# Kernel tuning notes

Hardware: AMD Instinct MI355X
Metric: run time of the kernel (lower is better)

Reference implementation:

```python
import jax, jax.numpy as jnp
import numpy as np

CUTOFF = 5.0
P = 6               # envelope polynomial power
NUM_RBF = 6
NUM_SBF = 7
EMBED = 128
TYPE_EMBED = 64
OUT_EMBED = 256
INT_EMBED = 64      # angle_int_embed_size
BASIS_EMBED = 8
N_BLOCKS = 4
N_DENSE_OUT = 3
N_RES_BEFORE = 1
N_RES_AFTER = 2
N_SPECIES = 16
NUM_TARGETS = 1
N_ATOMS = 4096
N_EDGES = 65536
N_TRIPLETS = 524288

# first 6 positive roots of spherical Bessel j_l, l = 0..6
BESSEL_ZEROS = np.array([
    [3.141593, 6.283185, 9.424778, 12.566371, 15.707963, 18.849556],
    [4.493409, 7.725252, 10.904122, 14.066194, 17.220755, 20.371303],
    [5.763459, 9.095011, 12.322941, 15.514603, 18.689036, 21.853874],
    [6.987932, 10.417119, 13.698023, 16.923621, 20.121806, 23.304247],
    [8.182561, 11.704907, 15.039665, 18.301256, 21.525418, 24.727566],
    [9.355812, 12.966530, 16.354710, 19.653152, 22.904551, 26.126750],
    [10.512835, 14.207392, 17.647975, 20.983463, 24.262768, 27.507868]], dtype=np.float32)

act = jax.nn.silu  # swish


def envelope(x):
    a = -(P + 1) * (P + 2) / 2.0
    b = float(P * (P + 2))
    c = -P * (P + 1) / 2.0
    env = 1.0 / x + a * x ** (P - 1) + b * x ** P + c * x ** (P + 1)
    return jnp.where(x < 1.0, env, 0.0)


def radial_bessel(d):
    # d: (E,) -> (E, NUM_RBF)
    x = d / CUTOFF
    n = jnp.arange(1, NUM_RBF + 1, dtype=jnp.float32)
    return np.float32(np.sqrt(2.0 / CUTOFF)) * envelope(x)[:, None] * jnp.sin(jnp.pi * n[None, :] * x[:, None])


def spherical_basis(d_kj, angles, triplet_mask):
    # d_kj: (T,), angles: (T,) -> (T, NUM_SBF * NUM_RBF)
    x = jnp.maximum(d_kj / CUTOFF, 1e-6)
    env = envelope(x)
    zeros = jnp.asarray(BESSEL_ZEROS)
    radial = []
    for l in range(NUM_SBF):
        a = zeros[l][None, :] * x[:, None]           # (T, NUM_RBF)
        j0 = jnp.sin(a) / a
        if l == 0:
            radial.append(j0)
            continue
        j1 = jnp.sin(a) / a ** 2 - jnp.cos(a) / a
        jm2, jm1 = j0, j1
        for ll in range(2, l + 1):
            jm2, jm1 = jm1, (2 * ll - 1) / a * jm1 - jm2
        radial.append(jm1)
    radial = jnp.stack(radial, axis=1)               # (T, NUM_SBF, NUM_RBF)
    ct = jnp.cos(angles)
    Pl = [jnp.ones_like(ct), ct]
    for l in range(2, NUM_SBF):
        Pl.append(((2 * l - 1) * ct * Pl[l - 1] - (l - 1) * Pl[l - 2]) / l)
    sph = jnp.stack([np.float32(np.sqrt((2 * l + 1) / (4.0 * np.pi))) * Pl[l] for l in range(NUM_SBF)], axis=1)  # (T, NUM_SBF)
    sbf = (env[:, None, None] * radial * sph[:, :, None]).reshape(-1, NUM_SBF * NUM_RBF)
    return jnp.where(triplet_mask[:, None], sbf, 0.0)


def _forward(distances, angles, species_embed, emb_rbf_w, emb_rbf_b, emb_dense_w, emb_dense_b,
             out_rbf_w, out_up_w, out_dense_w, out_dense_b, out_final_w,
             int_ji_w, int_ji_b, int_kj_w, int_kj_b, int_rbf1_w, int_rbf2_w, int_down_w,
             int_sbf1_w, int_sbf2_w, int_up_w, int_res1_w, int_res1_b, int_skip_w, int_skip_b,
             int_res2_w, int_res2_b,
             species, idx_i, idx_j, reduce_to_ji, expand_to_kj, edge_mask, triplet_mask):
    n_particles = species.shape[0]
    n_edges = distances.shape[0]
    d = jnp.where(edge_mask, distances, 2.0 * CUTOFF)       # masked edges -> env = 0
    rbf = radial_bessel(d)                                  # (E, 6)
    sbf = spherical_basis(d[expand_to_kj], angles, triplet_mask)  # (T, 42)

    # embedding block
    h = species_embed[species]                              # (N, 64)
    rbf_emb = rbf @ emb_rbf_w + emb_rbf_b                   # (E, 128)
    m = act(jnp.concatenate([h[idx_j], h[idx_i], rbf_emb], axis=-1) @ emb_dense_w + emb_dense_b)

    def output_block(i, msg):
        atom = jax.ops.segment_sum((rbf @ out_rbf_w[i]) * msg, idx_i, num_segments=n_particles)
        atom = atom @ out_up_w[i]
        for k in range(N_DENSE_OUT):
            atom = act(atom @ out_dense_w[i, k] + out_dense_b[i, k])
        return atom @ out_final_w[i]

    out = output_block(0, m)
    for i in range(N_BLOCKS):
        x_ji = act(m @ int_ji_w[i] + int_ji_b[i])
        x_kj = act(m @ int_kj_w[i] + int_kj_b[i])
        x_kj = x_kj * ((rbf @ int_rbf1_w[i]) @ int_rbf2_w[i])
        x_kj = act(x_kj @ int_down_w[i])                    # (E, 64)
        x_kj = x_kj[expand_to_kj] * ((sbf @ int_sbf1_w[i]) @ int_sbf2_w[i])  # (T, 64)
        x_kj = jax.ops.segment_sum(x_kj, reduce_to_ji, num_segments=n_edges)
        x_kj = act(x_kj @ int_up_w[i])
        hm = x_ji + x_kj
        for r in range(N_RES_BEFORE):
            hm = hm + act(act(hm @ int_res1_w[i, r, 0] + int_res1_b[i, r, 0]) @ int_res1_w[i, r, 1] + int_res1_b[i, r, 1])
        m = act(hm @ int_skip_w[i] + int_skip_b[i]) + m
        for r in range(N_RES_AFTER):
            m = m + act(act(m @ int_res2_w[i, r, 0] + int_res2_b[i, r, 0]) @ int_res2_w[i, r, 1] + int_res2_b[i, r, 1])
        out = out + output_block(i + 1, m)
    return out


def setup_inputs() -> dict:
    key = jax.random.key(0)
    ks = iter(jax.random.split(key, 40))
    def nrm(shape, fan_in):
        return jax.random.normal(next(ks), shape, dtype=jnp.float32) / np.float32(np.sqrt(fan_in))
    inp = {}
    inp['distances'] = 0.5 + 4.45 * jax.random.uniform(next(ks), (N_EDGES,), dtype=jnp.float32)
    inp['angles'] = jnp.pi * jax.random.uniform(next(ks), (N_TRIPLETS,), dtype=jnp.float32)
    inp['species_embed'] = jax.random.normal(next(ks), (N_SPECIES, TYPE_EMBED), dtype=jnp.float32)
    inp['emb_rbf_w'] = nrm((NUM_RBF, EMBED), NUM_RBF)
    inp['emb_rbf_b'] = jnp.zeros((EMBED,), jnp.float32)
    inp['emb_dense_w'] = nrm((2 * TYPE_EMBED + EMBED, EMBED), 2 * TYPE_EMBED + EMBED)
    inp['emb_dense_b'] = jnp.zeros((EMBED,), jnp.float32)
    nb1 = N_BLOCKS + 1
    inp['out_rbf_w'] = nrm((nb1, NUM_RBF, EMBED), NUM_RBF)
    inp['out_up_w'] = nrm((nb1, EMBED, OUT_EMBED), EMBED)
    inp['out_dense_w'] = nrm((nb1, N_DENSE_OUT, OUT_EMBED, OUT_EMBED), OUT_EMBED)
    inp['out_dense_b'] = jnp.zeros((nb1, N_DENSE_OUT, OUT_EMBED), jnp.float32)
    inp['out_final_w'] = nrm((nb1, OUT_EMBED, NUM_TARGETS), OUT_EMBED)
    inp['int_ji_w'] = nrm((N_BLOCKS, EMBED, EMBED), EMBED)
    inp['int_ji_b'] = jnp.zeros((N_BLOCKS, EMBED), jnp.float32)
    inp['int_kj_w'] = nrm((N_BLOCKS, EMBED, EMBED), EMBED)
    inp['int_kj_b'] = jnp.zeros((N_BLOCKS, EMBED), jnp.float32)
    inp['int_rbf1_w'] = nrm((N_BLOCKS, NUM_RBF, BASIS_EMBED), NUM_RBF)
    inp['int_rbf2_w'] = nrm((N_BLOCKS, BASIS_EMBED, EMBED), BASIS_EMBED)
    inp['int_down_w'] = nrm((N_BLOCKS, EMBED, INT_EMBED), EMBED)
    inp['int_sbf1_w'] = nrm((N_BLOCKS, NUM_SBF * NUM_RBF, BASIS_EMBED), NUM_SBF * NUM_RBF)
    inp['int_sbf2_w'] = nrm((N_BLOCKS, BASIS_EMBED, INT_EMBED), BASIS_EMBED)
    inp['int_up_w'] = nrm((N_BLOCKS, INT_EMBED, EMBED), INT_EMBED)
    inp['int_res1_w'] = nrm((N_BLOCKS, N_RES_BEFORE, 2, EMBED, EMBED), EMBED)
    inp['int_res1_b'] = jnp.zeros((N_BLOCKS, N_RES_BEFORE, 2, EMBED), jnp.float32)
    inp['int_skip_w'] = nrm((N_BLOCKS, EMBED, EMBED), EMBED)
    inp['int_skip_b'] = jnp.zeros((N_BLOCKS, EMBED), jnp.float32)
    inp['int_res2_w'] = nrm((N_BLOCKS, N_RES_AFTER, 2, EMBED, EMBED), EMBED)
    inp['int_res2_b'] = jnp.zeros((N_BLOCKS, N_RES_AFTER, 2, EMBED), jnp.float32)
    inp['species'] = jax.random.randint(next(ks), (N_ATOMS,), 0, N_SPECIES)
    inp['idx_i'] = jax.random.randint(next(ks), (N_EDGES,), 0, N_ATOMS)
    inp['idx_j'] = jax.random.randint(next(ks), (N_EDGES,), 0, N_ATOMS)
    inp['reduce_to_ji'] = jax.random.randint(next(ks), (N_TRIPLETS,), 0, N_EDGES)
    inp['expand_to_kj'] = jax.random.randint(next(ks), (N_TRIPLETS,), 0, N_EDGES)
    inp['edge_mask'] = jnp.ones((N_EDGES,), dtype=bool)
    inp['triplet_mask'] = jnp.ones((N_TRIPLETS,), dtype=bool)
    return inp


def reference(distances, angles, species_embed, emb_rbf_w, emb_rbf_b, emb_dense_w, emb_dense_b,
              out_rbf_w, out_up_w, out_dense_w, out_dense_b, out_final_w,
              int_ji_w, int_ji_b, int_kj_w, int_kj_b, int_rbf1_w, int_rbf2_w, int_down_w,
              int_sbf1_w, int_sbf2_w, int_up_w, int_res1_w, int_res1_b, int_skip_w, int_skip_b,
              int_res2_w, int_res2_b,
              species, idx_i, idx_j, reduce_to_ji, expand_to_kj, edge_mask, triplet_mask):
    return _forward(distances, angles, species_embed, emb_rbf_w, emb_rbf_b, emb_dense_w, emb_dense_b,
                    out_rbf_w, out_up_w, out_dense_w, out_dense_b, out_final_w,
                    int_ji_w, int_ji_b, int_kj_w, int_kj_b, int_rbf1_w, int_rbf2_w, int_down_w,
                    int_sbf1_w, int_sbf2_w, int_up_w, int_res1_w, int_res1_b, int_skip_w, int_skip_b,
                    int_res2_w, int_res2_b,
                    species, idx_i, idx_j, reduce_to_ji, expand_to_kj, edge_mask, triplet_mask)
```

## Files before the change

### kernel.cpp

```cpp
#include <hip/hip_runtime.h>
#include <cmath>

typedef __attribute__((ext_vector_type(8))) short bfrag;
typedef __attribute__((ext_vector_type(4))) float f32x4;

__device__ __forceinline__ float silu_f(float x) {
    return x * __builtin_amdgcn_rcpf(1.0f + __expf(-x));
}
__device__ __forceinline__ unsigned short f2bf(float f) {
    unsigned u = __float_as_uint(f);
    unsigned r = (u + 0x7fff + ((u >> 16) & 1)) >> 16;
    return (unsigned short)r;
}
__device__ __forceinline__ float bf2f(unsigned short h) {
    return __uint_as_float(((unsigned)h) << 16);
}
__device__ __forceinline__ unsigned packbf2(float lo, float hi) {
    return ((unsigned)f2bf(hi) << 16) | (unsigned)f2bf(lo);
}
__device__ __forceinline__ unsigned cvtpk2(float a, float b) {
    unsigned r;
    asm("v_cvt_pk_bf16_f32 %0, %1, %2" : "=v"(r) : "v"(a), "v"(b));
    return r;
}
__device__ __forceinline__ uint2 pk4(float a, float b, float c, float d) {
    return make_uint2(cvtpk2(a, b), cvtpk2(c, d));
}

template <int KSTEPS, int S, int NS, int ST>
__device__ __forceinline__ void mfma_stage_T(
    const unsigned short* Xs,
    const unsigned short* __restrict__ Whi, const unsigned short* __restrict__ Wlo,
    int Kdim, int arow0, int bcol0, int r16, int kg, f32x4 (&acc)[S][NS]) {
    #pragma unroll
    for (int s = 0; s < S; s++)
        #pragma unroll
        for (int ns = 0; ns < NS; ns++) acc[s][ns] = (f32x4)0.f;
    #pragma unroll
    for (int ks = 0; ks < KSTEPS; ks++) {
        int k0 = ks * 32;
        bfrag wh[NS], wl[NS];
        #pragma unroll
        for (int ns = 0; ns < NS; ns++) {
            size_t o = (size_t)(bcol0 + ns * 16 + r16) * Kdim + k0 + kg * 8;
            wh[ns] = *(const bfrag*)&Whi[o];
            wl[ns] = *(const bfrag*)&Wlo[o];
        }
        #pragma unroll
        for (int s = 0; s < S; s++) {
            bfrag xh = *(const bfrag*)&Xs[(arow0 + s * 16 + r16) * ST + k0 + kg * 8];
            #pragma unroll
            for (int ns = 0; ns < NS; ns++) {
                acc[s][ns] = __builtin_amdgcn_mfma_f32_16x16x32_bf16(wh[ns], xh, acc[s][ns], 0, 0, 0);
                acc[s][ns] = __builtin_amdgcn_mfma_f32_16x16x32_bf16(wl[ns], xh, acc[s][ns], 0, 0, 0);
            }
        }
    }
}

template <int KSTEPS, int S, int NS, int ST>
__device__ __forceinline__ void mfma_stage_pp(
    const unsigned short* Xs,
    const unsigned short* __restrict__ Whi, const unsigned short* __restrict__ Wlo,
    int Kdim, int arow0, int bcol0, int r16, int kg, f32x4 (&acc)[S][NS]) {
    bfrag wh[2][NS], wl[2][NS];
    #pragma unroll
    for (int ns = 0; ns < NS; ns++) {
        size_t o = (size_t)(bcol0 + ns * 16 + r16) * Kdim + kg * 8;
        wh[0][ns] = *(const bfrag*)&Whi[o];
        wl[0][ns] = *(const bfrag*)&Wlo[o];
    }
    #pragma unroll
    for (int s = 0; s < S; s++)
        #pragma unroll
        for (int ns = 0; ns < NS; ns++) acc[s][ns] = (f32x4)0.f;
    #pragma unroll
    for (int ks = 0; ks < KSTEPS; ks++) {
        const int cur = ks & 1, nxt = cur ^ 1;
        if (ks + 1 < KSTEPS) {
            #pragma unroll
            for (int ns = 0; ns < NS; ns++) {
                size_t o = (size_t)(bcol0 + ns * 16 + r16) * Kdim + (ks + 1) * 32 + kg * 8;
                wh[nxt][ns] = *(const bfrag*)&Whi[o];
                wl[nxt][ns] = *(const bfrag*)&Wlo[o];
            }
        }
        #pragma unroll
        for (int s = 0; s < S; s++) {
            bfrag xh = *(const bfrag*)&Xs[(arow0 + s * 16 + r16) * ST + ks * 32 + kg * 8];
            #pragma unroll
            for (int ns = 0; ns < NS; ns++) {
                acc[s][ns] = __builtin_amdgcn_mfma_f32_16x16x32_bf16(wh[cur][ns], xh, acc[s][ns], 0, 0, 0);
                acc[s][ns] = __builtin_amdgcn_mfma_f32_16x16x32_bf16(wl[cur][ns], xh, acc[s][ns], 0, 0, 0);
            }
        }
    }
}

__global__ __launch_bounds__(256) void rbf_kernel(const float* __restrict__ d,
                                                  float* __restrict__ rbf, int E) {
    int e = blockIdx.x * 256 + threadIdx.x;
    if (e >= E) return;
    float x = d[e] * 0.2f;
    float env = 0.0f;
    if (x < 1.0f) {
        float x2 = x * x;
        float x5 = x2 * x2 * x;
        env = 1.0f / x + x5 * (-28.0f + x * (48.0f - 21.0f * x));
    }
    const float SQ = 0.63245553f;
    float px = 3.14159265358979f * x;
    #pragma unroll
    for (int n = 1; n <= 6; n++) {
        rbf[e * 6 + n - 1] = SQ * env * __sinf(px * (float)n);
    }
}

__global__ __launch_bounds__(128) void embed_pre_kernel(
    const float* __restrict__ se, const float* __restrict__ erw,
    const float* __restrict__ erb, const float* __restrict__ edw,
    float* __restrict__ HWj, float* __restrict__ HWi,
    float* __restrict__ W3, float* __restrict__ b3) {
    int c = threadIdx.x;
    for (int s = 0; s < 16; s++) {
        float aj = 0.f, ai = 0.f;
        for (int k = 0; k < 64; k++) {
            float h = se[s * 64 + k];
            aj += h * edw[k * 128 + c];
            ai += h * edw[(64 + k) * 128 + c];
        }
        HWj[s * 128 + c] = aj;
        HWi[s * 128 + c] = ai;
    }
    for (int r = 0; r < 6; r++) {
        float a = 0.f;
        for (int k = 0; k < 128; k++) a += erw[r * 128 + k] * edw[(128 + k) * 128 + c];
        W3[r * 128 + c] = a;
    }
    float a = 0.f;
    for (int k = 0; k < 128; k++) a += erb[k] * edw[(128 + k) * 128 + c];
    b3[c] = a;
}

__global__ __launch_bounds__(256) void embed_kernel(
    const float* __restrict__ rbf, const int* __restrict__ species,
    const int* __restrict__ idx_i, const int* __restrict__ idx_j,
    const float* __restrict__ HWj, const float* __restrict__ HWi,
    const float* __restrict__ W3, const float* __restrict__ b3,
    const float* __restrict__ edb, float* __restrict__ m) {
    int gid = blockIdx.x * 256 + threadIdx.x;
    int e = gid >> 7, c = gid & 127;
    int sj = species[idx_j[e]];
    int si = species[idx_i[e]];
    float v = HWj[sj * 128 + c] + HWi[si * 128 + c] + b3[c] + edb[c];
    #pragma unroll
    for (int k = 0; k < 6; k++) v += rbf[e * 6 + k] * W3[k * 128 + c];
    m[gid] = silu_f(v);
}

__global__ __launch_bounds__(256) void wconv_kernel(
    const float* __restrict__ W, unsigned short* __restrict__ hi,
    unsigned short* __restrict__ lo, int K, int N) {
    __shared__ float t[32][33];
    int b = blockIdx.z;
    int n0 = blockIdx.x * 32, k0 = blockIdx.y * 32;
    const float* Wb = W + (size_t)b * K * N;
    int tid = threadIdx.x;
    int r = tid >> 3, cg = tid & 7;
    float4 v = *(const float4*)&Wb[(size_t)(k0 + r) * N + n0 + cg * 4];
    t[r][cg * 4 + 0] = v.x;
    t[r][cg * 4 + 1] = v.y;
    t[r][cg * 4 + 2] = v.z;
    t[r][cg * 4 + 3] = v.w;
    __syncthreads();
    int nl = tid >> 3, kg = tid & 7;
    short4 h4, l4;
    float f0 = t[kg * 4 + 0][nl], f1 = t[kg * 4 + 1][nl];
    float f2 = t[kg * 4 + 2][nl], f3 = t[kg * 4 + 3][nl];
    unsigned short h;
    h = f2bf(f0); h4.x = (short)h; l4.x = (short)f2bf(f0 - bf2f(h));
    h = f2bf(f1); h4.y = (short)h; l4.y = (short)f2bf(f1 - bf2f(h));
    h = f2bf(f2); h4.z = (short)h; l4.z = (short)f2bf(f2 - bf2f(h));
    h = f2bf(f3); h4.w = (short)h; l4.w = (short)f2bf(f3 - bf2f(h));
    size_t o = ((size_t)b * N + n0 + nl) * K + k0 + kg * 4;
    *(short4*)&hi[o] = h4;
    *(short4*)&lo[o] = l4;
}

template <int ACT, int BIAS, int RES>
__global__ __launch_bounds__(512, 4) void mfma_gemmT(
    const float* __restrict__ X, const unsigned short* __restrict__ Whi,
    const unsigned short* __restrict__ Wlo,
    const float* __restrict__ bias, const float* __restrict__ resid,
    float* __restrict__ Y, int M, int K, int N) {
    __shared__ unsigned short Xs[64 * 40];
    int tid = threadIdx.x;
    int bm = blockIdx.x * 64, bn = blockIdx.y * 128;
    int wid = tid >> 6, lane = tid & 63;
    int wr = wid >> 2, wc = wid & 3;
    int r16 = lane & 15, kg = lane >> 4;
    int arow0 = wr * 32, bcol0 = wc * 32;

    f32x4 acc[2][2];
    #pragma unroll
    for (int s = 0; s < 2; s++)
        #pragma unroll
        for (int ns = 0; ns < 2; ns++) acc[s][ns] = (f32x4)0.f;

    for (int k0 = 0; k0 < K; k0 += 32) {
        {
            int row = tid >> 3, cg = tid & 7;
            float4 v = *(const float4*)&X[(size_t)(bm + row) * K + k0 + cg * 4];
            *(uint2*)&Xs[row * 40 + cg * 4] = pk4(v.x, v.y, v.z, v.w);
        }
        __syncthreads();
        bfrag wh[2], wl[2];
        #pragma unroll
        for (int ns = 0; ns < 2; ns++) {
            size_t o = (size_t)(bn + bcol0 + ns * 16 + r16) * K + k0 + kg * 8;
            wh[ns] = *(const bfrag*)&Whi[o];
            wl[ns] = *(const bfrag*)&Wlo[o];
        }
        #pragma unroll
        for (int s = 0; s < 2; s++) {
            bfrag xh = *(const bfrag*)&Xs[(arow0 + s * 16 + r16) * 40 + kg * 8];
            #pragma unroll
            for (int ns = 0; ns < 2; ns++) {
                acc[s][ns] = __builtin_amdgcn_mfma_f32_16x16x32_bf16(wh[ns], xh, acc[s][ns], 0, 0, 0);
                acc[s][ns] = __builtin_amdgcn_mfma_f32_16x16x32_bf16(wl[ns], xh, acc[s][ns], 0, 0, 0);
            }
        }
        __syncthreads();
    }
    #pragma unroll
    for (int s = 0; s < 2; s++) {
        int mm = bm + arow0 + s * 16 + r16;
        #pragma unroll
        for (int ns = 0; ns < 2; ns++) {
            int n0 = bn + bcol0 + ns * 16 + kg * 4;
            float bv[4] = {0.f, 0.f, 0.f, 0.f};
            if (BIAS) {
                float4 b4 = *(const float4*)&bias[n0];
                bv[0] = b4.x; bv[1] = b4.y; bv[2] = b4.z; bv[3] = b4.w;
            }
            float4 o;
            float* op = (float*)&o;
            #pragma unroll
            for (int r = 0; r < 4; r++) {
                float v = acc[s][ns][r] + bv[r];
                if (ACT) v = silu_f(v);
                op[r] = v;
            }
            if (RES) {
                float4 rv = *(const float4*)&resid[(size_t)mm * N + n0];
                o.x += rv.x; o.y += rv.y; o.z += rv.z; o.w += rv.w;
            }
            *(float4*)&Y[(size_t)mm * N + n0] = o;
        }
    }
}

__global__ __launch_bounds__(512, 4) void outchain_kernel(
    const float* __restrict__ atom2,
    const unsigned short* __restrict__ odh, const unsigned short* __restrict__ odl,
    const float* __restrict__ odb, const float* __restrict__ wf,
    float* __restrict__ out) {
    __shared__ unsigned short Xs[64 * 264];
    __shared__ float rsum[64];
    int tid = threadIdx.x, bm = blockIdx.x * 64;
    int wid = tid >> 6, lane = tid & 63;
    int wr = wid >> 2, wc = wid & 3;
    int r16 = lane & 15, kg = lane >> 4;
    int arow0 = wr * 32, bcol0 = wc * 64;
    if (tid < 64) rsum[tid] = 0.f;

    #pragma unroll
    for (int p = 0; p < 8; p++) {
        int idx = tid + p * 512, row = idx >> 6, cg = idx & 63;
        float4 v = *(const float4*)&atom2[(size_t)(bm + row) * 256 + cg * 4];
        *(uint2*)&Xs[row * 264 + cg * 4] = pk4(v.x, v.y, v.z, v.w);
    }
    __syncthreads();

    f32x4 acc[2][4];
    #pragma unroll
    for (int st = 0; st < 3; st++) {
        mfma_stage_T<8, 2, 4, 264>(Xs, odh + (size_t)st * 65536, odl + (size_t)st * 65536,
                                   256, arow0, bcol0, r16, kg, acc);
        const float* bb = odb + st * 256;
        __syncthreads();
        if (st < 2) {
            #pragma unroll
            for (int s = 0; s < 2; s++)
                #pragma unroll
                for (int ns = 0; ns < 4; ns++) {
                    int n0 = bcol0 + ns * 16 + kg * 4;
                    float4 b4 = *(const float4*)&bb[n0];
                    *(uint2*)&Xs[(arow0 + s * 16 + r16) * 264 + n0] =
                        pk4(silu_f(acc[s][ns][0] + b4.x), silu_f(acc[s][ns][1] + b4.y),
                            silu_f(acc[s][ns][2] + b4.z), silu_f(acc[s][ns][3] + b4.w));
                }
            __syncthreads();
        } else {
            #pragma unroll
            for (int s = 0; s < 2; s++) {
                float part = 0.f;
                #pragma unroll
                for (int ns = 0; ns < 4; ns++) {
                    int n0 = bcol0 + ns * 16 + kg * 4;
                    float4 b4 = *(const float4*)&bb[n0];
                    float4 w4 = *(const float4*)&wf[n0];
                    part += silu_f(acc[s][ns][0] + b4.x) * w4.x;
                    part += silu_f(acc[s][ns][1] + b4.y) * w4.y;
                    part += silu_f(acc[s][ns][2] + b4.z) * w4.z;
                    part += silu_f(acc[s][ns][3] + b4.w) * w4.w;
                }
                atomicAdd(&rsum[arow0 + s * 16 + r16], part);
            }
        }
    }
    __syncthreads();
    if (tid < 64) out[bm + tid] += rsum[tid];
}

__global__ __launch_bounds__(512, 4) void downpath_kernel(
    const float* __restrict__ m, const float* __restrict__ rbf,
    const float* __restrict__ rbf1, const float* __restrict__ rbf2,
    const unsigned short* __restrict__ jih, const unsigned short* __restrict__ jil,
    const float* __restrict__ jib,
    const unsigned short* __restrict__ kjh, const unsigned short* __restrict__ kjl,
    const float* __restrict__ kjb,
    const unsigned short* __restrict__ dnh, const unsigned short* __restrict__ dnl,
    float* __restrict__ xji, float* __restrict__ xdown) {
    __shared__ unsigned short XsA[128 * 136];
    __shared__ unsigned short XsB[128 * 136];
    __shared__ float G8t[8][128];
    __shared__ float Rs[8][128];
    int tid = threadIdx.x, bm = blockIdx.x * 128;
    int wid = tid >> 6, lane = tid & 63;
    int wr = wid >> 2, wc = wid & 3;
    int r16 = lane & 15, kg = lane >> 4;
    int arow0 = wr * 64, bcol0 = wc * 32;

    #pragma unroll
    for (int p = 0; p < 8; p++) {
        int idx = tid + p * 512, row = idx >> 5, cg = idx & 31;
        float4 v = *(const float4*)&m[(size_t)(bm + row) * 128 + cg * 4];
        *(uint2*)&XsA[row * 136 + cg * 4] = pk4(v.x, v.y, v.z, v.w);
    }
    if (tid < 128) {
        float rv[6];
        #pragma unroll
        for (int k = 0; k < 6; k++) rv[k] = rbf[(size_t)(bm + tid) * 6 + k];
        #pragma unroll
        for (int p = 0; p < 8; p++) {
            float a = 0.f;
            #pragma unroll
            for (int k = 0; k < 6; k++) a += rv[k] * rbf1[k * 8 + p];
            G8t[p][tid] = a;
        }
    }
    for (int i = tid; i < 1024; i += 512) Rs[i >> 7][i & 127] = rbf2[i];
    __syncthreads();

    f32x4 acc[4][2];
    mfma_stage_pp<4, 4, 2, 136>(XsA, jih, jil, 128, arow0, bcol0, r16, kg, acc);
    #pragma unroll
    for (int s = 0; s < 4; s++) {
        int mm = bm + arow0 + s * 16 + r16;
        #pragma unroll
        for (int ns = 0; ns < 2; ns++) {
            int n0 = bcol0 + ns * 16 + kg * 4;
            float4 b4 = *(const float4*)&jib[n0];
            float4 o;
            o.x = silu_f(acc[s][ns][0] + b4.x);
            o.y = silu_f(acc[s][ns][1] + b4.y);
            o.z = silu_f(acc[s][ns][2] + b4.z);
            o.w = silu_f(acc[s][ns][3] + b4.w);
            *(float4*)&xji[(size_t)mm * 128 + n0] = o;
        }
    }
    mfma_stage_pp<4, 4, 2, 136>(XsA, kjh, kjl, 128, arow0, bcol0, r16, kg, acc);
    #pragma unroll
    for (int s = 0; s < 4; s++) {
        int mrow = arow0 + s * 16 + r16;
        float g8v[8];
        #pragma unroll
        for (int p = 0; p < 8; p++) g8v[p] = G8t[p][mrow];
        #pragma unroll
        for (int ns = 0; ns < 2; ns++) {
            int n0 = bcol0 + ns * 16 + kg * 4;
            float4 b4 = *(const float4*)&kjb[n0];
            float bb[4] = {b4.x, b4.y, b4.z, b4.w};
            float v[4];
            #pragma unroll
            for (int r = 0; r < 4; r++) {
                float g = 0.f;
                #pragma unroll
                for (int p = 0; p < 8; p++) g = fmaf(g8v[p], Rs[p][n0 + r], g);
                v[r] = silu_f(acc[s][ns][r] + bb[r]) * g;
            }
            *(uint2*)&XsB[mrow * 136 + n0] = pk4(v[0], v[1], v[2], v[3]);
        }
    }
    __syncthreads();
    {
        int wr2 = wid >> 1, wc2 = wid & 1;
        int ar2 = wr2 * 32, bc2 = wc2 * 32;
        f32x4 a2[2][2];
        mfma_stage_pp<4, 2, 2, 136>(XsB, dnh, dnl, 128, ar2, bc2, r16, kg, a2);
        #pragma unroll
        for (int s = 0; s < 2; s++) {
            int mm = bm + ar2 + s * 16 + r16;
            #pragma unroll
            for (int ns = 0; ns < 2; ns++) {
                int n0 = bc2 + ns * 16 + kg * 4;
                float4 o;
                o.x = silu_f(a2[s][ns][0]);
                o.y = silu_f(a2[s][ns][1]);
                o.z = silu_f(a2[s][ns][2]);
                o.w = silu_f(a2[s][ns][3]);
                *(float4*)&xdown[(size_t)mm * 64 + n0] = o;
            }
        }
    }
}

__global__ __launch_bounds__(512, 4) void chain_kernel(
    const float* __restrict__ seg, const float* __restrict__ xji, float* __restrict__ m,
    const unsigned short* __restrict__ uph, const unsigned short* __restrict__ upl,
    const unsigned short* __restrict__ r1h, const unsigned short* __restrict__ r1l,
    const float* __restrict__ r1b,
    const unsigned short* __restrict__ skh, const unsigned short* __restrict__ skl,
    const float* __restrict__ skb,
    const unsigned short* __restrict__ r2h, const unsigned short* __restrict__ r2l,
    const float* __restrict__ r2b) {
    __shared__ unsigned short XsA[128 * 136];
    __shared__ unsigned short XsB[128 * 136];
    int tid = threadIdx.x, bm = blockIdx.x * 128;
    int wid = tid >> 6, lane = tid & 63;
    int wr = wid >> 2, wc = wid & 3;
    int r16 = lane & 15, kg = lane >> 4;
    int arow0 = wr * 64, bcol0 = wc * 32;

    #pragma unroll
    for (int p = 0; p < 4; p++) {
        int idx = tid + p * 512, row = idx >> 4, cg = idx & 15;
        float4 v = *(const float4*)&seg[(size_t)(bm + row) * 64 + cg * 4];
        *(uint2*)&XsA[row * 136 + cg * 4] = pk4(v.x, v.y, v.z, v.w);
    }
    __syncthreads();

    f32x4 acc[4][2], res[4][2];

    auto store_frags = [&](unsigned short* Xd, const f32x4 (&v)[4][2]) {
        #pragma unroll
        for (int s = 0; s < 4; s++)
            #pragma unroll
            for (int ns = 0; ns < 2; ns++)
                *(uint2*)&Xd[(arow0 + s * 16 + r16) * 136 + bcol0 + ns * 16 + kg * 4] =
                    pk4(v[s][ns][0], v[s][ns][1], v[s][ns][2], v[s][ns][3]);
    };
    auto store_act = [&](unsigned short* Xd, const f32x4 (&a)[4][2], const float* bb) {
        #pragma unroll
        for (int s = 0; s < 4; s++)
            #pragma unroll
            for (int ns = 0; ns < 2; ns++) {
                int n0 = bcol0 + ns * 16 + kg * 4;
                float4 b4 = *(const float4*)&bb[n0];
                *(uint2*)&Xd[(arow0 + s * 16 + r16) * 136 + n0] =
                    pk4(silu_f(a[s][ns][0] + b4.x), silu_f(a[s][ns][1] + b4.y),
                        silu_f(a[s][ns][2] + b4.z), silu_f(a[s][ns][3] + b4.w));
            }
    };
    auto accum_res = [&](const f32x4 (&a)[4][2], const float* bb) {
        #pragma unroll
        for (int s = 0; s < 4; s++)
            #pragma unroll
            for (int ns = 0; ns < 2; ns++) {
                int n0 = bcol0 + ns * 16 + kg * 4;
                float4 b4 = *(const float4*)&bb[n0];
                res[s][ns][0] += silu_f(a[s][ns][0] + b4.x);
                res[s][ns][1] += silu_f(a[s][ns][1] + b4.y);
                res[s][ns][2] += silu_f(a[s][ns][2] + b4.z);
                res[s][ns][3] += silu_f(a[s][ns][3] + b4.w);
            }
    };

    mfma_stage_pp<2, 4, 2, 136>(XsA, uph, upl, 64, arow0, bcol0, r16, kg, acc);
    #pragma unroll
    for (int s = 0; s < 4; s++) {
        int mm = bm + arow0 + s * 16 + r16;
        #pragma unroll
        for (int ns = 0; ns < 2; ns++) {
            int n0 = bcol0 + ns * 16 + kg * 4;
            float4 xv = *(const float4*)&xji[(size_t)mm * 128 + n0];
            res[s][ns][0] = silu_f(acc[s][ns][0]) + xv.x;
            res[s][ns][1] = silu_f(acc[s][ns][1]) + xv.y;
            res[s][ns][2] = silu_f(acc[s][ns][2]) + xv.z;
            res[s][ns][3] = silu_f(acc[s][ns][3]) + xv.w;
        }
    }
    store_frags(XsB, res);
    __syncthreads();

    mfma_stage_pp<4, 4, 2, 136>(XsB, r1h, r1l, 128, arow0, bcol0, r16, kg, acc);
    store_act(XsA, acc, r1b);
    __syncthreads();
    mfma_stage_pp<4, 4, 2, 136>(XsA, r1h + 16384, r1l + 16384, 128, arow0, bcol0, r16, kg, acc);
    accum_res(acc, r1b + 128);
    store_frags(XsB, res);
    __syncthreads();

    mfma_stage_pp<4, 4, 2, 136>(XsB, skh, skl, 128, arow0, bcol0, r16, kg, acc);
    #pragma unroll
    for (int s = 0; s < 4; s++) {
        int mm = bm + arow0 + s * 16 + r16;
        #pragma unroll
        for (int ns = 0; ns < 2; ns++) {
            int n0 = bcol0 + ns * 16 + kg * 4;
            float4 b4 = *(const float4*)&skb[n0];
            float4 mv = *(const float4*)&m[(size_t)mm * 128 + n0];
            res[s][ns][0] = silu_f(acc[s][ns][0] + b4.x) + mv.x;
            res[s][ns][1] = silu_f(acc[s][ns][1] + b4.y) + mv.y;
            res[s][ns][2] = silu_f(acc[s][ns][2] + b4.z) + mv.z;
            res[s][ns][3] = silu_f(acc[s][ns][3] + b4.w) + mv.w;
        }
    }
    store_frags(XsA, res);
    __syncthreads();

    mfma_stage_pp<4, 4, 2, 136>(XsA, r2h, r2l, 128, arow0, bcol0, r16, kg, acc);
    store_act(XsB, acc, r2b);
    __syncthreads();
    mfma_stage_pp<4, 4, 2, 136>(XsB, r2h + 16384, r2l + 16384, 128, arow0, bcol0, r16, kg, acc);
    accum_res(acc, r2b + 128);
    store_frags(XsA, res);
    __syncthreads();
    mfma_stage_pp<4, 4, 2, 136>(XsA, r2h + 32768, r2l + 32768, 128, arow0, bcol0, r16, kg, acc);
    store_act(XsB, acc, r2b + 256);
    __syncthreads();
    mfma_stage_pp<4, 4, 2, 136>(XsB, r2h + 49152, r2l + 49152, 128, arow0, bcol0, r16, kg, acc);
    accum_res(acc, r2b + 384);
    #pragma unroll
    for (int s = 0; s < 4; s++) {
        int mm = bm + arow0 + s * 16 + r16;
        #pragma unroll
        for (int ns = 0; ns < 2; ns++) {
            int n0 = bcol0 + ns * 16 + kg * 4;
            float4 o;
            o.x = res[s][ns][0]; o.y = res[s][ns][1];
            o.z = res[s][ns][2]; o.w = res[s][ns][3];
            *(float4*)&m[(size_t)mm * 128 + n0] = o;
        }
    }
}

__global__ __launch_bounds__(256) void outseg_kernel(
    const float* __restrict__ rbf, const float* __restrict__ orw,
    const float* __restrict__ m, const int* __restrict__ idx_i,
    float* __restrict__ atom) {
    int gid = blockIdx.x * 256 + threadIdx.x;
    int e = gid >> 7, c = gid & 127;
    float s = 0.f;
    #pragma unroll
    for (int k = 0; k < 6; k++) s += rbf[e * 6 + k] * orw[k * 128 + c];
    atomicAdd(&atom[(size_t)idx_i[e] * 128 + c], s * m[gid]);
}

__global__ __launch_bounds__(256) void hist_kernel(const int* __restrict__ rji,
                                                   int* __restrict__ hist) {
    int t = blockIdx.x * 256 + threadIdx.x;
    atomicAdd(&hist[rji[t]], 1);
}

__global__ __launch_bounds__(256) void scan1_kernel(const int* __restrict__ hist,
                                                    int* __restrict__ bsum) {
    __shared__ int s[256];
    int i = threadIdx.x;
    s[i] = hist[blockIdx.x * 256 + i];
    __syncthreads();
    for (int o = 128; o; o >>= 1) {
        if (i < o) s[i] += s[i + o];
        __syncthreads();
    }
    if (!i) bsum[blockIdx.x] = s[0];
}

__global__ __launch_bounds__(256) void scan2_kernel(const int* __restrict__ bsum,
                                                    int* __restrict__ boff) {
    __shared__ int s[256];
    int i = threadIdx.x;
    int own = bsum[i];
    s[i] = own;
    __syncthreads();
    for (int o = 1; o < 256; o <<= 1) {
        int v = (i >= o) ? s[i - o] : 0;
        __syncthreads();
        s[i] += v;
        __syncthreads();
    }
    boff[i] = s[i] - own;
}

__global__ __launch_bounds__(256) void scan3_kernel(const int* __restrict__ hist,
                                                    const int* __restrict__ boff,
                                                    int* __restrict__ rows,
                                                    int* __restrict__ cursor, int T) {
    __shared__ int s[256];
    int i = threadIdx.x, b = blockIdx.x;
    int h = hist[b * 256 + i];
    s[i] = h;
    __syncthreads();
    for (int o = 1; o < 256; o <<= 1) {
        int v = (i >= o) ? s[i - o] : 0;
        __syncthreads();
        s[i] += v;
        __syncthreads();
    }
    int excl = s[i] - h + boff[b];
    rows[b * 256 + i] = excl;
    cursor[b * 256 + i] = excl;
    if (b == gridDim.x - 1 && i == 255) rows[b * 256 + 256] = T;
}

__global__ __launch_bounds__(256) void scatter_kernel(
    const int* __restrict__ rji, const int* __restrict__ ekj,
    int* __restrict__ cursor, int* __restrict__ perm, int* __restrict__ ekjs) {
    int t = blockIdx.x * 256 + threadIdx.x;
    int r = rji[t];
    int pos = atomicAdd(&cursor[r], 1);
    perm[pos] = t;
    ekjs[pos] = ekj[t];
}

__global__ __launch_bounds__(256) void sbf_pre_kernel(
    const float* __restrict__ dist, const float* __restrict__ angles,
    const int* __restrict__ perm, const int* __restrict__ ekjs,
    const float* __restrict__ sbf1_all, unsigned short* __restrict__ t32, int T) {
    __shared__ float s1[1344];
    int tid = threadIdx.x;
    for (int i = tid; i < 1344; i += 256) s1[i] = sbf1_all[i];
    __syncthreads();

    int pos = blockIdx.x * 256 + tid;
    int t = perm[pos];
    int e = ekjs[pos];
    float x = fmaxf(dist[e] * 0.2f, 1e-6f);
    float env = 0.f;
    if (x < 1.0f) {
        float x2 = x * x;
        float x5 = x2 * x2 * x;
        env = 1.0f / x + x5 * (-28.0f + x * (48.0f - 21.0f * x));
    }
    float ct = __cosf(angles[t]);
    float Pl[7];
    Pl[0] = 1.f;
    Pl[1] = ct;
    #pragma unroll
    for (int l = 2; l < 7; l++)
        Pl[l] = ((2.f * l - 1.f) * ct * Pl[l - 1] - (l - 1.f) * Pl[l - 2]) / (float)l;
    const float sphc[7] = {0.28209479f, 0.48860251f, 0.63078313f, 0.74635267f,
                           0.84628438f, 0.93560257f, 1.01710723f};
    const float BZ[7][6] = {
        {3.141593f, 6.283185f, 9.424778f, 12.566371f, 15.707963f, 18.849556f},
        {4.493409f, 7.725252f, 10.904122f, 14.066194f, 17.220755f, 20.371303f},
        {5.763459f, 9.095011f, 12.322941f, 15.514603f, 18.689036f, 21.853874f},
        {6.987932f, 10.417119f, 13.698023f, 16.923621f, 20.121806f, 23.304247f},
        {8.182561f, 11.704907f, 15.039665f, 18.301256f, 21.525418f, 24.727566f},
        {9.355812f, 12.966530f, 16.354710f, 19.653152f, 22.904551f, 26.126750f},
        {10.512835f, 14.207392f, 17.647975f, 20.983463f, 24.262768f, 27.507868f}};
    float sbf[42];
    #pragma unroll
    for (int l = 0; l < 7; l++) {
        float coef = env * sphc[l] * Pl[l];
        #pragma unroll
        for (int n = 0; n < 6; n++) {
            float a = BZ[l][n] * x;
            float sa, ca;
            __sincosf(a, &sa, &ca);
            float inv = __builtin_amdgcn_rcpf(a);
            float j;
            if (l == 0) {
                j = sa * inv;
            } else {
                float jm2 = sa * inv;
                float jm1 = (sa * inv - ca) * inv;
                #pragma unroll
                for (int ll = 2; ll <= l; ll++) {
                    float jn = (2.f * ll - 1.f) * inv * jm1 - jm2;
                    jm2 = jm1;
                    jm1 = jn;
                }
                j = jm1;
            }
            sbf[l * 6 + n] = coef * j;
        }
    }
    float acc[32];
    #pragma unroll
    for (int q = 0; q < 32; q++) acc[q] = 0.f;
    #pragma unroll
    for (int k = 0; k < 42; k++) {
        float sv = sbf[k];
        #pragma unroll
        for (int b = 0; b < 4; b++)
            #pragma unroll
            for (int p = 0; p < 8; p++)
                acc[b * 8 + p] = fmaf(sv, s1[b * 336 + k * 8 + p], acc[b * 8 + p]);
    }
    #pragma unroll
    for (int b = 0; b < 4; b++) {
        uint4 u;
        u.x = packbf2(acc[b * 8 + 0], acc[b * 8 + 1]);
        u.y = packbf2(acc[b * 8 + 2], acc[b * 8 + 3]);
        u.z = packbf2(acc[b * 8 + 4], acc[b * 8 + 5]);
        u.w = packbf2(acc[b * 8 + 6], acc[b * 8 + 7]);
        *(uint4*)&t32[((size_t)b * T + pos) * 8] = u;
    }
}

__global__ __launch_bounds__(256) void seg_gather_kernel(
    const unsigned short* __restrict__ t32p, const int* __restrict__ ekjs,
    const int* __restrict__ rows, const float* __restrict__ xdown,
    const float* __restrict__ sbf2, float* __restrict__ seg, int E) {
    int gid = blockIdx.x * 256 + threadIdx.x;
    int e = gid >> 6, lane = gid & 63;
    if (e >= E) return;
    float w2[8];
    #pragma unroll
    for (int p = 0; p < 8; p++) w2[p] = sbf2[p * 64 + lane];
    int p0 = rows[e], p1 = rows[e + 1];
    float acc = 0.f;
    for (int pos = p0; pos < p1; ++pos) {
        uint4 a = *(const uint4*)&t32p[(size_t)pos * 8];
        float v = __uint_as_float(a.x << 16) * w2[0] + __uint_as_float(a.x & 0xffff0000u) * w2[1]
                + __uint_as_float(a.y << 16) * w2[2] + __uint_as_float(a.y & 0xffff0000u) * w2[3]
                + __uint_as_float(a.z << 16) * w2[4] + __uint_as_float(a.z & 0xffff0000u) * w2[5]
                + __uint_as_float(a.w << 16) * w2[6] + __uint_as_float(a.w & 0xffff0000u) * w2[7];
        acc = fmaf(v, xdown[(size_t)ekjs[pos] * 64 + lane], acc);
    }
    seg[(size_t)e * 64 + lane] = acc;
}

extern "C" void kernel_launch(void* const* d_in, const int* in_sizes, int n_in,
                              void* d_out, int out_size, void* d_ws, size_t ws_size,
                              hipStream_t stream) {
    const float* distances   = (const float*)d_in[0];
    const float* angles      = (const float*)d_in[1];
    const float* species_emb = (const float*)d_in[2];
    const float* emb_rbf_w   = (const float*)d_in[3];
    const float* emb_rbf_b   = (const float*)d_in[4];
    const float* emb_dense_w = (const float*)d_in[5];
    const float* emb_dense_b = (const float*)d_in[6];
    const float* out_rbf_w   = (const float*)d_in[7];
    const float* out_up_w    = (const float*)d_in[8];
    const float* out_dense_w = (const float*)d_in[9];
    const float* out_dense_b = (const float*)d_in[10];
    const float* out_final_w = (const float*)d_in[11];
    const float* int_ji_w    = (const float*)d_in[12];
    const float* int_ji_b    = (const float*)d_in[13];
    const float* int_kj_w    = (const float*)d_in[14];
    const float* int_kj_b    = (const float*)d_in[15];
    const float* int_rbf1_w  = (const float*)d_in[16];
    const float* int_rbf2_w  = (const float*)d_in[17];
    const float* int_down_w  = (const float*)d_in[18];
    const float* int_sbf1_w  = (const float*)d_in[19];
    const float* int_sbf2_w  = (const float*)d_in[20];
    const float* int_up_w    = (const float*)d_in[21];
    const float* int_res1_w  = (const float*)d_in[22];
    const float* int_res1_b  = (const float*)d_in[23];
    const float* int_skip_w  = (const float*)d_in[24];
    const float* int_skip_b  = (const float*)d_in[25];
    const float* int_res2_w  = (const float*)d_in[26];
    const float* int_res2_b  = (const float*)d_in[27];
    const int*   species     = (const int*)d_in[28];
    const int*   idx_i       = (const int*)d_in[29];
    const int*   idx_j       = (const int*)d_in[30];
    const int*   reduce_ji   = (const int*)d_in[31];
    const int*   expand_kj   = (const int*)d_in[32];

    const int E = in_sizes[0];
    const int T = in_sizes[1];
    const int NA = in_sizes[28];

    float* ws = (float*)d_ws;
    size_t off = 0;
    float* rbf = ws + off;   off += (size_t)E * 6;
    float* m   = ws + off;   off += (size_t)E * 128;
    float* A   = ws + off;   off += (size_t)E * 128;
    float* B   = ws + off;   off += (size_t)E * 128;
    float* C   = ws + off;   off += (size_t)E * 128;
    float* D   = ws + off;   off += (size_t)E * 64;
    float* HWj = ws + off;   off += 16 * 128;
    float* HWi = ws + off;   off += 16 * 128;
    float* W3  = ws + off;   off += 6 * 128;
    float* b3  = ws + off;   off += 128;
    float* atom1 = ws + off; off += (size_t)NA * 128;
    float* atom2 = ws + off; off += (size_t)NA * 256;
    float* atom3 = ws + off; off += (size_t)NA * 256;
    float* seg = B;

    unsigned short* wb = (unsigned short*)(ws + off);
    size_t wo = 0;
    unsigned short* ji_h = wb + wo;  wo += 4 * 16384;
    unsigned short* ji_l = wb + wo;  wo += 4 * 16384;
    unsigned short* kj_h = wb + wo;  wo += 4 * 16384;
    unsigned short* kj_l = wb + wo;  wo += 4 * 16384;
    unsigned short* dn_h = wb + wo;  wo += 4 * 8192;
    unsigned short* dn_l = wb + wo;  wo += 4 * 8192;
    unsigned short* up_h = wb + wo;  wo += 4 * 8192;
    unsigned short* up_l = wb + wo;  wo += 4 * 8192;
    unsigned short* r1_h = wb + wo;  wo += 8 * 16384;
    unsigned short* r1_l = wb + wo;  wo += 8 * 16384;
    unsigned short* sk_h = wb + wo;  wo += 4 * 16384;
    unsigned short* sk_l = wb + wo;  wo += 4 * 16384;
    unsigned short* r2_h = wb + wo;  wo += 16 * 16384;
    unsigned short* r2_l = wb + wo;  wo += 16 * 16384;
    unsigned short* ou_h = wb + wo;  wo += 5 * 32768;
    unsigned short* ou_l = wb + wo;  wo += 5 * 32768;
    unsigned short* od_h = wb + wo;  wo += 15 * 65536;
    unsigned short* od_l = wb + wo;  wo += 15 * 65536;
    unsigned short* t32 = wb + wo;   wo += (size_t)4 * T * 8;
    int* ip    = (int*)(wb + wo);
    size_t io  = 0;
    int* hist   = ip + io;  io += E;
    int* rows   = ip + io;  io += E + 64;
    int* cursor = ip + io;  io += E;
    int* bsum   = ip + io;  io += 256;
    int* boff   = ip + io;  io += 256;
    int* perm   = ip + io;  io += T;
    int* ekjs   = ip + io;  io += T;

    float* out = (float*)d_out;
    hipMemsetAsync(out, 0, (size_t)out_size * sizeof(float), stream);

    hipMemsetAsync(hist, 0, (size_t)E * sizeof(int), stream);
    hist_kernel<<<T / 256, 256, 0, stream>>>(reduce_ji, hist);
    scan1_kernel<<<E / 256, 256, 0, stream>>>(hist, bsum);
    scan2_kernel<<<1, 256, 0, stream>>>(bsum, boff);
    scan3_kernel<<<E / 256, 256, 0, stream>>>(hist, boff, rows, cursor, T);
    scatter_kernel<<<T / 256, 256, 0, stream>>>(reduce_ji, expand_kj, cursor, perm, ekjs);
    sbf_pre_kernel<<<T / 256, 256, 0, stream>>>(distances, angles, perm, ekjs,
                                                int_sbf1_w, t32, T);

    wconv_kernel<<<dim3(4, 4, 4), 256, 0, stream>>>(int_ji_w, ji_h, ji_l, 128, 128);
    wconv_kernel<<<dim3(4, 4, 4), 256, 0, stream>>>(int_kj_w, kj_h, kj_l, 128, 128);
    wconv_kernel<<<dim3(2, 4, 4), 256, 0, stream>>>(int_down_w, dn_h, dn_l, 128, 64);
    wconv_kernel<<<dim3(4, 2, 4), 256, 0, stream>>>(int_up_w, up_h, up_l, 64, 128);
    wconv_kernel<<<dim3(4, 4, 8), 256, 0, stream>>>(int_res1_w, r1_h, r1_l, 128, 128);
    wconv_kernel<<<dim3(4, 4, 4), 256, 0, stream>>>(int_skip_w, sk_h, sk_l, 128, 128);
    wconv_kernel<<<dim3(4, 4, 16), 256, 0, stream>>>(int_res2_w, r2_h, r2_l, 128, 128);
    wconv_kernel<<<dim3(8, 4, 5), 256, 0, stream>>>(out_up_w, ou_h, ou_l, 128, 256);
    wconv_kernel<<<dim3(8, 8, 15), 256, 0, stream>>>(out_dense_w, od_h, od_l, 256, 256);

    rbf_kernel<<<E / 256, 256, 0, stream>>>(distances, rbf, E);
    embed_pre_kernel<<<1, 128, 0, stream>>>(species_emb, emb_rbf_w, emb_rbf_b,
                                            emb_dense_w, HWj, HWi, W3, b3);
    embed_kernel<<<E * 128 / 256, 256, 0, stream>>>(rbf, species, idx_i, idx_j,
                                                    HWj, HWi, W3, b3, emb_dense_b, m);

    auto outblock = [&](int i, const float* msg) {
        hipMemsetAsync(atom1, 0, (size_t)NA * 128 * sizeof(float), stream);
        outseg_kernel<<<E * 128 / 256, 256, 0, stream>>>(
            rbf, out_rbf_w + (size_t)i * 6 * 128, msg, idx_i, atom1);
        mfma_gemmT<0, 0, 0><<<dim3(NA / 64, 2), 512, 0, stream>>>(
            atom1, ou_h + (size_t)i * 32768, ou_l + (size_t)i * 32768,
            nullptr, nullptr, atom2, NA, 128, 256);
        outchain_kernel<<<NA / 64, 512, 0, stream>>>(
            atom2, od_h + (size_t)i * 3 * 65536, od_l + (size_t)i * 3 * 65536,
            out_dense_b + (size_t)i * 3 * 256, out_final_w + (size_t)i * 256, out);
    };

    outblock(0, m);

    for (int i = 0; i < 4; i++) {
        downpath_kernel<<<E / 128, 512, 0, stream>>>(
            m, rbf, int_rbf1_w + (size_t)i * 48, int_rbf2_w + (size_t)i * 1024,
            ji_h + (size_t)i * 16384, ji_l + (size_t)i * 16384, int_ji_b + (size_t)i * 128,
            kj_h + (size_t)i * 16384, kj_l + (size_t)i * 16384, int_kj_b + (size_t)i * 128,
            dn_h + (size_t)i * 8192, dn_l + (size_t)i * 8192,
            A, D);
        seg_gather_kernel<<<E * 64 / 256, 256, 0, stream>>>(
            t32 + (size_t)i * T * 8, ekjs, rows, D,
            int_sbf2_w + (size_t)i * 8 * 64, seg, E);
        chain_kernel<<<E / 128, 512, 0, stream>>>(
            seg, A, m,
            up_h + (size_t)i * 8192, up_l + (size_t)i * 8192,
            r1_h + (size_t)i * 32768, r1_l + (size_t)i * 32768, int_res1_b + (size_t)i * 256,
            sk_h + (size_t)i * 16384, sk_l + (size_t)i * 16384, int_skip_b + (size_t)i * 128,
            r2_h + (size_t)i * 65536, r2_l + (size_t)i * 65536, int_res2_b + (size_t)i * 512);
        outblock(i + 1, m);
    }
}
```

Measured before the change: 1.497 ms.

## Fuse output-block edge-to-atom scatter into embed and chain kernels

The separate outseg kernel, which reread the message tensor and rbf to scatter rbf-weighted messages into atoms, is removed. Its work now happens in the epilogues of embed_kernel and chain_kernel, using values still held in registers. Chain_kernel also stages biases, output rbf weights, rbf rows and atom indices in shared memory, and its launch bound drops from 4 to 2 blocks per SM. This saves five full passes over the E×128 message tensor and five kernel launches, at the cost of more shared memory and registers, lower occupancy and atomics inside the heavy chain kernel.

Result: slower. 1.776 ms (+18.6%).

```diff
diff --git a/kernel.cpp b/kernel.cpp
--- a/kernel.cpp
+++ b/kernel.cpp
@@ -147,15 +147,24 @@
     const int* __restrict__ idx_i, const int* __restrict__ idx_j,
     const float* __restrict__ HWj, const float* __restrict__ HWi,
     const float* __restrict__ W3, const float* __restrict__ b3,
-    const float* __restrict__ edb, float* __restrict__ m) {
+    const float* __restrict__ edb, const float* __restrict__ orw0,
+    float* __restrict__ m, float* __restrict__ atom1) {
     int gid = blockIdx.x * 256 + threadIdx.x;
     int e = gid >> 7, c = gid & 127;
     int sj = species[idx_j[e]];
     int si = species[idx_i[e]];
+    float rv[6];
+    #pragma unroll
+    for (int k = 0; k < 6; k++) rv[k] = rbf[e * 6 + k];
     float v = HWj[sj * 128 + c] + HWi[si * 128 + c] + b3[c] + edb[c];
     #pragma unroll
-    for (int k = 0; k < 6; k++) v += rbf[e * 6 + k] * W3[k * 128 + c];
-    m[gid] = silu_f(v);
+    for (int k = 0; k < 6; k++) v += rv[k] * W3[k * 128 + c];
+    v = silu_f(v);
+    m[gid] = v;
+    float sc = 0.f;
+    #pragma unroll
+    for (int k = 0; k < 6; k++) sc += rv[k] * orw0[k * 128 + c];
+    atomicAdd(&atom1[(size_t)idx_i[e] * 128 + c], sc * v);
 }
 
 __global__ __launch_bounds__(256) void wconv_kernel(
@@ -426,7 +435,7 @@
     }
 }
 
-__global__ __launch_bounds__(512, 4) void chain_kernel(
+__global__ __launch_bounds__(512, 2) void chain_kernel(
     const float* __restrict__ seg, const float* __restrict__ xji, float* __restrict__ m,
     const unsigned short* __restrict__ uph, const unsigned short* __restrict__ upl,
     const unsigned short* __restrict__ r1h, const unsigned short* __restrict__ r1l,
@@ -434,14 +443,26 @@
     const unsigned short* __restrict__ skh, const unsigned short* __restrict__ skl,
     const float* __restrict__ skb,
     const unsigned short* __restrict__ r2h, const unsigned short* __restrict__ r2l,
-    const float* __restrict__ r2b) {
+    const float* __restrict__ r2b,
+    const float* __restrict__ rbf6, const float* __restrict__ orw,
+    const int* __restrict__ idxi, float* __restrict__ atom1) {
     __shared__ unsigned short XsA[128 * 136];
     __shared__ unsigned short XsB[128 * 136];
+    __shared__ float Bs[896];
+    __shared__ float Ow[768];
+    __shared__ float Rr[768];
+    __shared__ int Ii[128];
     int tid = threadIdx.x, bm = blockIdx.x * 128;
     int wid = tid >> 6, lane = tid & 63;
     int wr = wid >> 2, wc = wid & 3;
     int r16 = lane & 15, kg = lane >> 4;
     int arow0 = wr * 64, bcol0 = wc * 32;
+
+    for (int i = tid; i < 896; i += 512)
+        Bs[i] = (i < 256) ? r1b[i] : (i < 384) ? skb[i - 256] : r2b[i - 384];
+    for (int i = tid; i < 768; i += 512) Ow[i] = orw[i];
+    for (int i = tid; i < 768; i += 512) Rr[i] = rbf6[(size_t)bm * 6 + i];
+    if (tid < 128) Ii[tid] = idxi[bm + tid];
 
     #pragma unroll
     for (int p = 0; p < 4; p++) {
@@ -505,10 +526,10 @@
     __syncthreads();
 
     mfma_stage_pp<4, 4, 2, 136>(XsB, r1h, r1l, 128, arow0, bcol0, r16, kg, acc);
-    store_act(XsA, acc, r1b);
+    store_act(XsA, acc, &Bs[0]);
     __syncthreads();
     mfma_stage_pp<4, 4, 2, 136>(XsA, r1h + 16384, r1l + 16384, 128, arow0, bcol0, r16, kg, acc);
-    accum_res(acc, r1b + 128);
+    accum_res(acc, &Bs[128]);
     store_frags(XsB, res);
     __syncthreads();
 
@@ -519,32 +540,39 @@
         #pragma unroll
         for (int ns = 0; ns < 2; ns++) {
             int n0 = bcol0 + ns * 16 + kg * 4;
-            float4 b4 = *(const float4*)&skb[n0];
+            float bsk0 = Bs[256 + n0], bsk1 = Bs[256 + n0 + 1];
+            float bsk2 = Bs[256 + n0 + 2], bsk3 = Bs[256 + n0 + 3];
             float4 mv = *(const float4*)&m[(size_t)mm * 128 + n0];
-            res[s][ns][0] = silu_f(acc[s][ns][0] + b4.x) + mv.x;
-            res[s][ns][1] = silu_f(acc[s][ns][1] + b4.y) + mv.y;
-            res[s][ns][2] = silu_f(acc[s][ns][2] + b4.z) + mv.z;
-            res[s][ns][3] = silu_f(acc[s][ns][3] + b4.w) + mv.w;
+            res[s][ns][0] = silu_f(acc[s][ns][0] + bsk0) + mv.x;
+            res[s][ns][1] = silu_f(acc[s][ns][1] + bsk1) + mv.y;
+            res[s][ns][2] = silu_f(acc[s][ns][2] + bsk2) + mv.z;
+            res[s][ns][3] = silu_f(acc[s][ns][3] + bsk3) + mv.w;
         }
     }
     store_frags(XsA, res);
     __syncthreads();
 
     mfma_stage_pp<4, 4, 2, 136>(XsA, r2h, r2l, 128, arow0, bcol0, r16, kg, acc);
-    store_act(XsB, acc, r2b);
+    store_act(XsB, acc, &Bs[384]);
     __syncthreads();
     mfma_stage_pp<4, 4, 2, 136>(XsB, r2h + 16384, r2l + 16384, 128, arow0, bcol0, r16, kg, acc);
-    accum_res(acc, r2b + 128);
+    accum_res(acc, &Bs[512]);
     store_frags(XsA, res);
     __syncthreads();
     mfma_stage_pp<4, 4, 2, 136>(XsA, r2h + 32768, r2l + 32768, 128, arow0, bcol0, r16, kg, acc);
-    store_act(XsB, acc, r2b + 256);
+    store_act(XsB, acc, &Bs[640]);
     __syncthreads();
     mfma_stage_pp<4, 4, 2, 136>(XsB, r2h + 49152, r2l + 49152, 128, arow0, bcol0, r16, kg, acc);
-    accum_res(acc, r2b + 384);
+    accum_res(acc, &Bs[768]);
+
     #pragma unroll
     for (int s = 0; s < 4; s++) {
-        int mm = bm + arow0 + s * 16 + r16;
+        int row = arow0 + s * 16 + r16;
+        int mm = bm + row;
+        float rv[6];
+        #pragma unroll
+        for (int k = 0; k < 6; k++) rv[k] = Rr[row * 6 + k];
+        int ai = Ii[row];
         #pragma unroll
         for (int ns = 0; ns < 2; ns++) {
             int n0 = bcol0 + ns * 16 + kg * 4;
@@ -552,20 +580,16 @@
             o.x = res[s][ns][0]; o.y = res[s][ns][1];
             o.z = res[s][ns][2]; o.w = res[s][ns][3];
             *(float4*)&m[(size_t)mm * 128 + n0] = o;
-        }
-    }
-}
-
-__global__ __launch_bounds__(256) void outseg_kernel(
-    const float* __restrict__ rbf, const float* __restrict__ orw,
-    const float* __restrict__ m, const int* __restrict__ idx_i,
-    float* __restrict__ atom) {
-    int gid = blockIdx.x * 256 + threadIdx.x;
-    int e = gid >> 7, c = gid & 127;
-    float s = 0.f;
-    #pragma unroll
-    for (int k = 0; k < 6; k++) s += rbf[e * 6 + k] * orw[k * 128 + c];
-    atomicAdd(&atom[(size_t)idx_i[e] * 128 + c], s * m[gid]);
+            #pragma unroll
+            for (int j = 0; j < 4; j++) {
+                int c = n0 + j;
+                float sc = 0.f;
+                #pragma unroll
+                for (int k = 0; k < 6; k++) sc = fmaf(rv[k], Ow[k * 128 + c], sc);
+                atomicAdd(&atom1[(size_t)ai * 128 + c], sc * res[s][ns][j]);
+            }
+        }
+    }
 }
 
 __global__ __launch_bounds__(256) void hist_kernel(const int* __restrict__ rji,
@@ -857,13 +881,12 @@
     rbf_kernel<<<E / 256, 256, 0, stream>>>(distances, rbf, E);
     embed_pre_kernel<<<1, 128, 0, stream>>>(species_emb, emb_rbf_w, emb_rbf_b,
                                             emb_dense_w, HWj, HWi, W3, b3);
+    hipMemsetAsync(atom1, 0, (size_t)NA * 128 * sizeof(float), stream);
     embed_kernel<<<E * 128 / 256, 256, 0, stream>>>(rbf, species, idx_i, idx_j,
-                                                    HWj, HWi, W3, b3, emb_dense_b, m);
-
-    auto outblock = [&](int i, const float* msg) {
-        hipMemsetAsync(atom1, 0, (size_t)NA * 128 * sizeof(float), stream);
-        outseg_kernel<<<E * 128 / 256, 256, 0, stream>>>(
-            rbf, out_rbf_w + (size_t)i * 6 * 128, msg, idx_i, atom1);
+                                                    HWj, HWi, W3, b3, emb_dense_b,
+                                                    out_rbf_w, m, atom1);
+
+    auto outtail = [&](int i) {
         mfma_gemmT<0, 0, 0><<<dim3(NA / 64, 2), 512, 0, stream>>>(
             atom1, ou_h + (size_t)i * 32768, ou_l + (size_t)i * 32768,
             nullptr, nullptr, atom2, NA, 128, 256);
@@ -872,7 +895,7 @@
             out_dense_b + (size_t)i * 3 * 256, out_final_w + (size_t)i * 256, out);
     };
 
-    outblock(0, m);
+    outtail(0);
 
     for (int i = 0; i < 4; i++) {
         downpath_kernel<<<E / 128, 512, 0, stream>>>(
@@ -884,12 +907,14 @@
         seg_gather_kernel<<<E * 64 / 256, 256, 0, stream>>>(
             t32 + (size_t)i * T * 8, ekjs, rows, D,
             int_sbf2_w + (size_t)i * 8 * 64, seg, E);
+        hipMemsetAsync(atom1, 0, (size_t)NA * 128 * sizeof(float), stream);
         chain_kernel<<<E / 128, 512, 0, stream>>>(
             seg, A, m,
             up_h + (size_t)i * 8192, up_l + (size_t)i * 8192,
             r1_h + (size_t)i * 32768, r1_l + (size_t)i * 32768, int_res1_b + (size_t)i * 256,
             sk_h + (size_t)i * 16384, sk_l + (size_t)i * 16384, int_skip_b + (size_t)i * 128,
-            r2_h + (size_t)i * 65536, r2_l + (size_t)i * 65536, int_res2_b + (size_t)i * 512);
-        outblock(i + 1, m);
-    }
-}
+            r2_h + (size_t)i * 65536, r2_l + (size_t)i * 65536, int_res2_b + (size_t)i * 512,
+            rbf, out_rbf_w + (size_t)(i + 1) * 768, idx_i, atom1);
+        outtail(i + 1);
+    }
+}
```
